# Kernel tuning notes

Hardware: AMD Instinct MI355X
Metric: run time of the kernel (lower is better)

Reference implementation:

```python
import jax, jax.numpy as jnp
import numpy as np

K = 16            # neighbors
RATIO = 0.25      # sampling ratio
BN_EPS = 1e-5


def setup_inputs() -> dict:
    key = jax.random.key(0)
    k1, k2, k3 = jax.random.split(key, 3)
    B, N, Cin, Cout = 8, 8192, 64, 128
    x = jax.random.normal(k1, (B, N, Cin), dtype=jnp.float32)
    p1 = jax.random.uniform(k2, (B, N, 3), dtype=jnp.float32)
    W = jax.random.normal(k3, (Cout, Cin), dtype=jnp.float32) * 0.05  # Conv1d(k=1, bias=False)
    gamma = jnp.ones((Cout,), dtype=jnp.float32)   # BatchNorm1d weight
    beta = jnp.zeros((Cout,), dtype=jnp.float32)   # BatchNorm1d bias
    return {"x": x, "p1": p1, "W": W, "gamma": gamma, "beta": beta}


def furthest_point_sample(p, M):
    """Greedy FPS. p: (B,N,3) -> (B,M) int32 indices. Starts at index 0 (CUDA impl convention)."""
    B, N, _ = p.shape
    first = jnp.zeros((B,), dtype=jnp.int32)
    mind = jnp.full((B, N), 1e10, dtype=p.dtype)

    def step(carry, _):
        mind, last = carry
        lp = jnp.take_along_axis(p, last[:, None, None].astype(jnp.int32), axis=1)  # (B,1,3)
        d = jnp.sum((p - lp) ** 2, axis=-1)          # (B,N)
        mind = jnp.minimum(mind, d)
        nxt = jnp.argmax(mind, axis=1).astype(jnp.int32)
        return (mind, nxt), nxt

    (_, _), rest = jax.lax.scan(step, (mind, first), None, length=M - 1)  # rest: (M-1,B)
    idx = jnp.concatenate([first[None, :], rest], axis=0)  # (M,B)
    return idx.T  # (B,M)


def reference(x, p1, W, gamma, beta):
    B, N, Cin = x.shape
    M = int(N * RATIO)

    # --- FPS sampling + gather coords ---
    fps_idx = furthest_point_sample(p1, M)                      # (B,M)
    p2 = jnp.take_along_axis(p1, fps_idx[:, :, None], axis=1)   # (B,M,3)

    # --- brute-force kNN of p1 around each p2 query ---
    d2 = (jnp.sum(p2 ** 2, -1)[:, :, None]
          - 2.0 * jnp.einsum('bmd,bnd->bmn', p2, p1)
          + jnp.sum(p1 ** 2, -1)[:, None, :])                   # (B,M,N)
    _, nbr = jax.lax.top_k(-d2, K)                              # (B,M,K) indices into N

    # --- shared MLP: 1x1 conv (no bias) + BatchNorm1d (training-mode stats) + ReLU ---
    h = jnp.einsum('bnc,oc->bno', x, W)                         # (B,N,Cout)
    mean = jnp.mean(h, axis=(0, 1))
    var = jnp.var(h, axis=(0, 1))
    h = (h - mean) * jax.lax.rsqrt(var + BN_EPS) * gamma + beta
    h = jax.nn.relu(h)

    # --- gather k neighbors per sampled point, max-pool over neighborhood ---
    feats = h[jnp.arange(B)[:, None, None], nbr]                # (B,M,K,Cout)
    y = jnp.max(feats, axis=2)                                  # (B,M,Cout)
    return y, p2
```

## Files before the change

kernel.cpp:

```cpp
#include <hip/hip_runtime.h>
#include <stdint.h>

#define Bb   8
#define Nn   8192
#define CIN  64
#define COUT 128
#define Mm   2048
#define KNN  16
#define NTOT (Bb*Nn)

typedef unsigned long long ull;
typedef float v2f __attribute__((ext_vector_type(2)));


__device__ __forceinline__ v2f pk_add(v2f a, v2f b)
{ v2f d; asm("v_pk_add_f32 %0, %1, %2" : "=v"(d) : "v"(a), "v"(b)); return d; }
__device__ __forceinline__ v2f pk_mul(v2f a, v2f b)
{ v2f d; asm("v_pk_mul_f32 %0, %1, %2" : "=v"(d) : "v"(a), "v"(b)); return d; }

__device__ __forceinline__ float wave_max16(float x)
{
    int v = __float_as_int(x), t;
    t = __builtin_amdgcn_update_dpp(v, v, 0x111, 0xf, 0xf, false);
    v = __float_as_int(fmaxf(__int_as_float(v), __int_as_float(t)));
    t = __builtin_amdgcn_update_dpp(v, v, 0x112, 0xf, 0xf, false);
    v = __float_as_int(fmaxf(__int_as_float(v), __int_as_float(t)));
    t = __builtin_amdgcn_update_dpp(v, v, 0x114, 0xf, 0xf, false);
    v = __float_as_int(fmaxf(__int_as_float(v), __int_as_float(t)));
    t = __builtin_amdgcn_update_dpp(v, v, 0x118, 0xf, 0xf, false);
    v = __float_as_int(fmaxf(__int_as_float(v), __int_as_float(t)));
    unsigned r0 = (unsigned)__builtin_amdgcn_readlane(v, 15);
    unsigned r1 = (unsigned)__builtin_amdgcn_readlane(v, 31);
    unsigned r2 = (unsigned)__builtin_amdgcn_readlane(v, 47);
    unsigned r3 = (unsigned)__builtin_amdgcn_readlane(v, 63);
    unsigned m0 = r0 > r1 ? r0 : r1;
    unsigned m1 = r2 > r3 ? r2 : r3;
    unsigned mm = m0 > m1 ? m0 : m1;
    return __uint_as_float(mm);
}

__global__ __launch_bounds__(256, 1)
void fps_kernel(const float* __restrict__ p1, float* __restrict__ p2out)
{
    __shared__ float px[Nn], py[Nn], pz[Nn];
    __shared__ alignas(16) ull wkey[2][4];
    const int b    = blockIdx.x;
    const int tid  = threadIdx.x;
    const int lane = tid & 63, wid = tid >> 6;
    const float* pb = p1 + b * Nn * 3;

    for (int i = tid; i < Nn * 3; i += 256) {
        float v = pb[i];
        int pt = i / 3;
        int c  = i - pt * 3;
        if (c == 0) px[pt] = v; else if (c == 1) py[pt] = v; else pz[pt] = v;
    }
    __syncthreads();

    v2f ppx[16], ppy[16], ppz[16], mind[16];
#pragma unroll
    for (int i = 0; i < 16; ++i) {
        int j0 = tid * 32 + 2 * i;
        ppx[i] = (v2f){px[j0], px[j0 + 1]};
        ppy[i] = (v2f){py[j0], py[j0 + 1]};
        ppz[i] = (v2f){pz[j0], pz[j0 + 1]};
        mind[i] = (v2f){1e10f, 1e10f};
    }

    float lx = px[0], ly = py[0], lz = pz[0];
    if (tid == 0) {
        int o = (b * Mm) * 3;
        p2out[o] = lx; p2out[o + 1] = ly; p2out[o + 2] = lz;
    }

    for (int m = 1; m < Mm; ++m) {
        const int buf = m & 1;
        float nx = -lx, ny = -ly, nz = -lz;
        v2f nx2 = (v2f){nx, nx}, ny2 = (v2f){ny, ny}, nz2 = (v2f){nz, nz};
        float bv0 = -1.0f, bv1 = -1.0f; int bj0 = 0, bj1 = 1;
#pragma unroll
        for (int i = 0; i < 16; ++i) {
            v2f dx = pk_add(ppx[i], nx2);
            v2f dy = pk_add(ppy[i], ny2);
            v2f dz = pk_add(ppz[i], nz2);
            v2f s  = pk_add(pk_add(pk_mul(dx, dx), pk_mul(dy, dy)),
                            pk_mul(dz, dz));
            float m0 = fminf(mind[i].x, s.x);
            float m1 = fminf(mind[i].y, s.y);
            mind[i].x = m0; mind[i].y = m1;
            if (m0 > bv0) { bv0 = m0; bj0 = 2 * i; }
            if (m1 > bv1) { bv1 = m1; bj1 = 2 * i + 1; }
        }
        float bestv; int bestj;
        if (bv1 > bv0 || (bv1 == bv0 && bj1 < bj0)) { bestv = bv1; bestj = bj1; }
        else                                        { bestv = bv0; bestj = bj0; }
        bestj += tid * 32;

        float wv = wave_max16(bestv);
        ull tie = __ballot(bestv == wv);
        int low = __ffsll((long long)tie) - 1;
        if (lane == low) {
            wkey[buf][wid] = ((ull)__float_as_uint(wv) << 32) |
                             (unsigned int)(~(unsigned int)bestj);
        }
        __syncthreads();

        ull k0 = wkey[buf][0], k1 = wkey[buf][1];
        ull k2 = wkey[buf][2], k3 = wkey[buf][3];
        ull k01 = k0 > k1 ? k0 : k1;
        ull k23 = k2 > k3 ? k2 : k3;
        ull fk  = k01 > k23 ? k01 : k23;
        int jw = (int)(~(unsigned int)fk);
        lx = px[jw]; ly = py[jw]; lz = pz[jw];
        if (tid == 0) {
            int o = (b * Mm + m) * 3;
            p2out[o] = lx; p2out[o + 1] = ly; p2out[o + 2] = lz;
        }
    }
}

__device__ __forceinline__ ull d2key(
    float qx, float qy, float qz, float qn, float x, float y, float z, int j)
{
    float dot = __fadd_rn(__fadd_rn(__fmul_rn(qx, x), __fmul_rn(qy, y)),
                          __fmul_rn(qz, z));
    float cn  = __fadd_rn(__fadd_rn(__fmul_rn(x, x), __fmul_rn(y, y)),
                          __fmul_rn(z, z));
    float d2  = __fadd_rn(__fsub_rn(qn, __fadd_rn(dot, dot)), cn);
    unsigned int bits = __float_as_uint(d2);
    unsigned int u = bits ^ (((unsigned int)((int)bits >> 31)) | 0x80000000u);
    return ((ull)u << 32) | (unsigned int)j;
}

__global__ __launch_bounds__(1024, 1)
void topk_kernel(const float* __restrict__ p1, const float* __restrict__ p2o,
                 int* __restrict__ nbr)
{
    __shared__ float px[Nn], py[Nn], pz[Nn];
    const int tid   = threadIdx.x;
    const int b     = blockIdx.x >> 7;
    const int mbase = (blockIdx.x & 127) << 4;
    const float* pb = p1 + b * Nn * 3;

    for (int i = tid; i < Nn * 3; i += 1024) {
        float v = pb[i];
        int pt = i / 3;
        int c  = i - pt * 3;
        if (c == 0) px[pt] = v; else if (c == 1) py[pt] = v; else pz[pt] = v;
    }
    __syncthreads();

    const int wid = tid >> 6, lane = tid & 63;
    const int qrow = b * Mm + mbase + wid;
    float qx = p2o[qrow * 3], qy = p2o[qrow * 3 + 1], qz = p2o[qrow * 3 + 2];
    float qn = __fadd_rn(__fadd_rn(__fmul_rn(qx, qx), __fmul_rn(qy, qy)),
                         __fmul_rn(qz, qz));

    const ull INV = ~0ull;
    ull k1 = INV, k2 = INV, k3 = INV;
#pragma unroll 4
    for (int i = 0; i < 128; ++i) {
        int j = lane + (i << 6);
        ull key = d2key(qx, qy, qz, qn, px[j], py[j], pz[j], j);
        bool b1 = key < k1, b2 = key < k2, b3 = key < k3;
        ull n1 = b1 ? key : k1;
        ull n2 = b1 ? k1 : (b2 ? key : k2);
        ull n3 = b2 ? k2 : (b3 ? key : k3);
        k1 = n1; k2 = n2; k3 = n3;
    }

    int* out = nbr + qrow * KNN;
    for (int r = 0; r < KNN; ++r) {
        ull wk = k1;
#pragma unroll
        for (int off = 1; off < 64; off <<= 1) {
            ull ok = __shfl_xor(wk, off, 64);
            wk = ok < wk ? ok : wk;
        }
        if (lane == 0) out[r] = (int)(unsigned int)(wk & 0xFFFFFFFFull);
        if (k1 == wk) { k1 = k2; k2 = k3; k3 = INV; }
        if (k1 == INV) {
            for (int i = 0; i < 128; ++i) {
                int j = lane + (i << 6);
                ull key = d2key(qx, qy, qz, qn, px[j], py[j], pz[j], j);
                if (key > wk) {
                    bool b1 = key < k1, b2 = key < k2, b3 = key < k3;
                    ull n1 = b1 ? key : k1;
                    ull n2 = b1 ? k1 : (b2 ? key : k2);
                    ull n3 = b2 ? k2 : (b3 ? key : k3);
                    k1 = n1; k2 = n2; k3 = n3;
                }
            }
        }
    }
}

__global__ __launch_bounds__(256)
void gemm_kernel(const float* __restrict__ x, const float* __restrict__ W,
                 float* __restrict__ h)
{
    const int r0 = blockIdx.x * 16 + (threadIdx.x >> 6) * 4;
    const int cp = threadIdx.x & 63;
    const float4* xp = (const float4*)(x + r0 * CIN);
    const float4* w0 = (const float4*)(W + (cp * 2) * CIN);
    const float4* w1 = (const float4*)(W + (cp * 2 + 1) * CIN);
    float a[4][2];
#pragma unroll
    for (int r = 0; r < 4; ++r) { a[r][0] = 0.f; a[r][1] = 0.f; }
#pragma unroll
    for (int k = 0; k < CIN / 4; ++k) {
        float4 wa = w0[k], wb = w1[k];
#pragma unroll
        for (int r = 0; r < 4; ++r) {
            float4 xv = xp[r * 16 + k];
            a[r][0] = fmaf(xv.x, wa.x, fmaf(xv.y, wa.y, fmaf(xv.z, wa.z, fmaf(xv.w, wa.w, a[r][0]))));
            a[r][1] = fmaf(xv.x, wb.x, fmaf(xv.y, wb.y, fmaf(xv.z, wb.z, fmaf(xv.w, wb.w, a[r][1]))));
        }
    }
#pragma unroll
    for (int r = 0; r < 4; ++r)
        *(float2*)(h + (r0 + r) * COUT + cp * 2) = make_float2(a[r][0], a[r][1]);
}

__global__ __launch_bounds__(256)
void stats_kernel(const float* __restrict__ h, float* __restrict__ stats)
{
    __shared__ float4 rs[256], rq[256];
    const int tid  = threadIdx.x;
    const int c4   = (tid & 31) * 4;
    const int rsub = tid >> 5;
    const int rbase = blockIdx.x * 256;
    float4 s = make_float4(0, 0, 0, 0), q = make_float4(0, 0, 0, 0);
    for (int i = 0; i < 32; ++i) {
        int r = rbase + rsub + i * 8;
        float4 v = *(const float4*)(h + r * COUT + c4);
        s.x += v.x; s.y += v.y; s.z += v.z; s.w += v.w;
        q.x = fmaf(v.x, v.x, q.x); q.y = fmaf(v.y, v.y, q.y);
        q.z = fmaf(v.z, v.z, q.z); q.w = fmaf(v.w, v.w, q.w);
    }
    rs[tid] = s; rq[tid] = q;
    __syncthreads();
    if (tid < 32) {
        for (int j = 1; j < 8; ++j) {
            float4 o = rs[tid + 32 * j];
            s.x += o.x; s.y += o.y; s.z += o.z; s.w += o.w;
            float4 oq = rq[tid + 32 * j];
            q.x += oq.x; q.y += oq.y; q.z += oq.z; q.w += oq.w;
        }
        atomicAdd(&stats[c4 + 0], s.x); atomicAdd(&stats[c4 + 1], s.y);
        atomicAdd(&stats[c4 + 2], s.z); atomicAdd(&stats[c4 + 3], s.w);
        atomicAdd(&stats[128 + c4 + 0], q.x); atomicAdd(&stats[128 + c4 + 1], q.y);
        atomicAdd(&stats[128 + c4 + 2], q.z); atomicAdd(&stats[128 + c4 + 3], q.w);
    }
}

__global__ void finalize_kernel(const float* __restrict__ stats,
                                const float* __restrict__ gamma,
                                const float* __restrict__ beta,
                                float* __restrict__ sb)
{
    int c = threadIdx.x;
    float mean = stats[c] * (1.0f / 65536.0f);
    float var  = stats[128 + c] * (1.0f / 65536.0f) - mean * mean;
    float scale = gamma[c] / sqrtf(var + 1e-5f);
    float bias  = beta[c] - mean * scale;
    sb[c] = scale; sb[128 + c] = bias;
}

__global__ __launch_bounds__(256)
void gather_kernel(const float* __restrict__ h, const int* __restrict__ nbr,
                   const float* __restrict__ sb, float* __restrict__ y)
{
    const int wid = threadIdx.x >> 6, lane = threadIdx.x & 63;
    const int t4 = blockIdx.x * 4 + wid;
    const int b  = t4 >> 11;
    const int c0 = lane * 2;
    float s0 = sb[c0], s1 = sb[c0 + 1];
    float b0 = sb[128 + c0], b1 = sb[128 + c0 + 1];
    const int* nb = nbr + t4 * KNN;
    float a0 = -1e30f, a1 = -1e30f;
#pragma unroll
    for (int k = 0; k < KNN; ++k) {
        int idx = nb[k];
        float2 v = *(const float2*)(h + ((b << 13) + idx) * COUT + c0);
        a0 = fmaxf(a0, fmaf(v.x, s0, b0));
        a1 = fmaxf(a1, fmaf(v.y, s1, b1));
    }
    a0 = fmaxf(a0, 0.0f); a1 = fmaxf(a1, 0.0f);
    *(float2*)(y + t4 * COUT + c0) = make_float2(a0, a1);
}

extern "C" void kernel_launch(void* const* d_in, const int* in_sizes, int n_in,
                              void* d_out, int out_size, void* d_ws, size_t ws_size,
                              hipStream_t stream)
{
    const float* x     = (const float*)d_in[0];
    const float* p1    = (const float*)d_in[1];
    const float* W     = (const float*)d_in[2];
    const float* gamma = (const float*)d_in[3];
    const float* beta  = (const float*)d_in[4];

    float* y  = (float*)d_out;
    float* p2 = (float*)d_out + Bb * Mm * COUT;

    char*  ws    = (char*)d_ws;
    float* h     = (float*)ws;
    int*   nbr   = (int*)(ws + 33619968);
    float* stats = (float*)(ws + 35717120);
    float* sb    = (float*)(ws + 35718144);

    hipMemsetAsync(stats, 0, 1024, stream);
    fps_kernel<<<Bb, 256, 0, stream>>>(p1, p2);
    gemm_kernel<<<NTOT / 16, 256, 0, stream>>>(x, W, h);
    stats_kernel<<<256, 256, 0, stream>>>(h, stats);
    finalize_kernel<<<1, 128, 0, stream>>>(stats, gamma, beta, sb);
    topk_kernel<<<Bb * 128, 1024, 0, stream>>>(p1, p2, nbr);
    gather_kernel<<<Bb * Mm / 4, 256, 0, stream>>>(h, nbr, sb, y);
}
```

Before: 2.293 ms.

## Fuse FPS with GEMM launch, widen FPS to 512 threads, replace barrier with tagged spin

FPS and the 1x1-conv GEMM now run in one launch: the first 8 blocks do FPS and the rest do the GEMM, so the GEMM fills idle CUs during the serial FPS. FPS uses 512 threads with half the points each, which shortens the per-iteration scan. The per-iteration __syncthreads is replaced by tagged 64-bit keys in volatile shared memory that each wave polls until all 8 waves have posted the current iteration. The spin-wait depends on waves being co-resident and on the tag/value packing fitting in 64 bits, and FPS blocks may now wait behind GEMM blocks for scheduling.

```diff
diff --git a/kernel.cpp b/kernel.cpp
--- a/kernel.cpp
+++ b/kernel.cpp
@@ -39,17 +39,46 @@
     return __uint_as_float(mm);
 }
 
-__global__ __launch_bounds__(256, 1)
-void fps_kernel(const float* __restrict__ p1, float* __restrict__ p2out)
+__global__ __launch_bounds__(512, 1)
+void fps_gemm_kernel(const float* __restrict__ p1, float* __restrict__ p2out,
+                     const float* __restrict__ x, const float* __restrict__ W,
+                     float* __restrict__ h)
 {
     __shared__ float px[Nn], py[Nn], pz[Nn];
-    __shared__ alignas(16) ull wkey[2][4];
+    __shared__ volatile ull wkey[2][8];
+    const int tid = threadIdx.x;
+
+    if (blockIdx.x >= 8) {
+        const int r0 = (blockIdx.x - 8) * 32 + (tid >> 6) * 4;
+        const int cp = tid & 63;
+        const float4* xp = (const float4*)(x + r0 * CIN);
+        const float4* w0 = (const float4*)(W + (cp * 2) * CIN);
+        const float4* w1 = (const float4*)(W + (cp * 2 + 1) * CIN);
+        float a[4][2];
+#pragma unroll
+        for (int r = 0; r < 4; ++r) { a[r][0] = 0.f; a[r][1] = 0.f; }
+#pragma unroll
+        for (int k = 0; k < CIN / 4; ++k) {
+            float4 wa = w0[k], wb = w1[k];
+#pragma unroll
+            for (int r = 0; r < 4; ++r) {
+                float4 xv = xp[r * 16 + k];
+                a[r][0] = fmaf(xv.x, wa.x, fmaf(xv.y, wa.y, fmaf(xv.z, wa.z, fmaf(xv.w, wa.w, a[r][0]))));
+                a[r][1] = fmaf(xv.x, wb.x, fmaf(xv.y, wb.y, fmaf(xv.z, wb.z, fmaf(xv.w, wb.w, a[r][1]))));
+            }
+        }
+#pragma unroll
+        for (int r = 0; r < 4; ++r)
+            *(float2*)(h + (r0 + r) * COUT + cp * 2) = make_float2(a[r][0], a[r][1]);
+        return;
+    }
+
     const int b    = blockIdx.x;
-    const int tid  = threadIdx.x;
     const int lane = tid & 63, wid = tid >> 6;
     const float* pb = p1 + b * Nn * 3;
 
-    for (int i = tid; i < Nn * 3; i += 256) {
+    if (tid < 16) ((volatile ull*)&wkey[0][0])[tid] = 0;
+    for (int i = tid; i < Nn * 3; i += 512) {
         float v = pb[i];
         int pt = i / 3;
         int c  = i - pt * 3;
@@ -57,10 +86,10 @@
     }
     __syncthreads();
 
-    v2f ppx[16], ppy[16], ppz[16], mind[16];
-#pragma unroll
-    for (int i = 0; i < 16; ++i) {
-        int j0 = tid * 32 + 2 * i;
+    v2f ppx[8], ppy[8], ppz[8], mind[8];
+#pragma unroll
+    for (int i = 0; i < 8; ++i) {
+        int j0 = tid * 16 + 2 * i;
         ppx[i] = (v2f){px[j0], px[j0 + 1]};
         ppy[i] = (v2f){py[j0], py[j0 + 1]};
         ppz[i] = (v2f){pz[j0], pz[j0 + 1]};
@@ -79,7 +108,7 @@
         v2f nx2 = (v2f){nx, nx}, ny2 = (v2f){ny, ny}, nz2 = (v2f){nz, nz};
         float bv0 = -1.0f, bv1 = -1.0f; int bj0 = 0, bj1 = 1;
 #pragma unroll
-        for (int i = 0; i < 16; ++i) {
+        for (int i = 0; i < 8; ++i) {
             v2f dx = pk_add(ppx[i], nx2);
             v2f dy = pk_add(ppy[i], ny2);
             v2f dz = pk_add(ppz[i], nz2);
@@ -94,23 +123,30 @@
         float bestv; int bestj;
         if (bv1 > bv0 || (bv1 == bv0 && bj1 < bj0)) { bestv = bv1; bestj = bj1; }
         else                                        { bestv = bv0; bestj = bj0; }
-        bestj += tid * 32;
+        bestj += tid * 16;
 
         float wv = wave_max16(bestv);
         ull tie = __ballot(bestv == wv);
         int low = __ffsll((long long)tie) - 1;
+        const ull tagv = (ull)m << 53;
         if (lane == low) {
-            wkey[buf][wid] = ((ull)__float_as_uint(wv) << 32) |
-                             (unsigned int)(~(unsigned int)bestj);
-        }
-        __syncthreads();
-
-        ull k0 = wkey[buf][0], k1 = wkey[buf][1];
-        ull k2 = wkey[buf][2], k3 = wkey[buf][3];
-        ull k01 = k0 > k1 ? k0 : k1;
-        ull k23 = k2 > k3 ? k2 : k3;
-        ull fk  = k01 > k23 ? k01 : k23;
-        int jw = (int)(~(unsigned int)fk);
+            wkey[buf][wid] = tagv | ((ull)__float_as_uint(wv) << 21) |
+                             (ull)(8191 - bestj);
+        }
+
+        ull k[8], mn;
+        do {
+#pragma unroll
+            for (int w = 0; w < 8; ++w) k[w] = wkey[buf][w];
+            mn = k[0];
+#pragma unroll
+            for (int w = 1; w < 8; ++w) mn = k[w] < mn ? k[w] : mn;
+        } while (mn < tagv);
+        ull fk = k[0];
+#pragma unroll
+        for (int w = 1; w < 8; ++w) fk = k[w] > fk ? k[w] : fk;
+
+        int jw = 8191 - (int)(fk & 0x1FFFFF);
         lx = px[jw]; ly = py[jw]; lz = pz[jw];
         if (tid == 0) {
             int o = (b * Mm + m) * 3;
@@ -196,33 +232,6 @@
 }
 
 __global__ __launch_bounds__(256)
-void gemm_kernel(const float* __restrict__ x, const float* __restrict__ W,
-                 float* __restrict__ h)
-{
-    const int r0 = blockIdx.x * 16 + (threadIdx.x >> 6) * 4;
-    const int cp = threadIdx.x & 63;
-    const float4* xp = (const float4*)(x + r0 * CIN);
-    const float4* w0 = (const float4*)(W + (cp * 2) * CIN);
-    const float4* w1 = (const float4*)(W + (cp * 2 + 1) * CIN);
-    float a[4][2];
-#pragma unroll
-    for (int r = 0; r < 4; ++r) { a[r][0] = 0.f; a[r][1] = 0.f; }
-#pragma unroll
-    for (int k = 0; k < CIN / 4; ++k) {
-        float4 wa = w0[k], wb = w1[k];
-#pragma unroll
-        for (int r = 0; r < 4; ++r) {
-            float4 xv = xp[r * 16 + k];
-            a[r][0] = fmaf(xv.x, wa.x, fmaf(xv.y, wa.y, fmaf(xv.z, wa.z, fmaf(xv.w, wa.w, a[r][0]))));
-            a[r][1] = fmaf(xv.x, wb.x, fmaf(xv.y, wb.y, fmaf(xv.z, wb.z, fmaf(xv.w, wb.w, a[r][1]))));
-        }
-    }
-#pragma unroll
-    for (int r = 0; r < 4; ++r)
-        *(float2*)(h + (r0 + r) * COUT + cp * 2) = make_float2(a[r][0], a[r][1]);
-}
-
-__global__ __launch_bounds__(256)
 void stats_kernel(const float* __restrict__ h, float* __restrict__ stats)
 {
     __shared__ float4 rs[256], rq[256];
@@ -310,8 +319,7 @@
     float* sb    = (float*)(ws + 35718144);
 
     hipMemsetAsync(stats, 0, 1024, stream);
-    fps_kernel<<<Bb, 256, 0, stream>>>(p1, p2);
-    gemm_kernel<<<NTOT / 16, 256, 0, stream>>>(x, W, h);
+    fps_gemm_kernel<<<8 + NTOT / 32, 512, 0, stream>>>(p1, p2, x, W, h);
     stats_kernel<<<256, 256, 0, stream>>>(h, stats);
     finalize_kernel<<<1, 128, 0, stream>>>(stats, gamma, beta, sb);
     topk_kernel<<<Bb * 128, 1024, 0, stream>>>(p1, p2, nbr);
```

Result: slower. 3.089 ms (+34.7%).
